# Kernel tuning notes

Measured on AMD Instinct MI355X. Metric: run time of the kernel, lower is better.

## Reference

```python
import jax, jax.numpy as jnp
import numpy as np

N_NODES = 100000
N_EDGES = 1600000
IN_DIM = 128
OUT_DIM = 32
N_HEADS = 4


def setup_inputs() -> dict:
    key = jax.random.key(0)
    k1, k2, k3, k4, k5 = jax.random.split(key, 5)
    x = jax.random.normal(k1, (N_NODES, IN_DIM), dtype=jnp.float32)
    edge_index = jax.random.randint(k2, (2, N_EDGES), 0, N_NODES, dtype=jnp.int64)
    # torch nn.Linear weight layout: [out_features, in_features]
    W = jax.random.normal(k3, (OUT_DIM * N_HEADS, IN_DIM), dtype=jnp.float32) * (1.0 / np.sqrt(IN_DIM))
    a_left = jax.random.normal(k4, (N_HEADS, OUT_DIM), dtype=jnp.float32) * 0.01
    a_right = jax.random.normal(k5, (N_HEADS, OUT_DIM), dtype=jnp.float32) * 0.01
    return {"x": x, "edge_index": edge_index, "W": W, "a_left": a_left, "a_right": a_right}


def reference(x, edge_index, W, a_left, a_right):
    N = x.shape[0]
    H, D = a_left.shape
    # h: [N, H, D]
    h = (x @ W.T).reshape(N, H, D)
    src = edge_index[0]
    dst = edge_index[1]
    h_src = h[src]                                   # [E, H, D] gather
    h_dst = h[dst]                                   # [E, H, D] gather
    e = jnp.einsum('ehd,hd->eh', h_src, a_left) + jnp.einsum('ehd,hd->eh', h_dst, a_right)
    e = jax.nn.leaky_relu(e, negative_slope=0.2)
    e_exp = jnp.exp(e)                               # faithful: no max-subtraction, as in source
    denom = jax.ops.segment_sum(e_exp, dst, num_segments=N)   # [N, H]
    alpha = e_exp / (denom[dst] + 1e-8)              # [E, H]
    weighted = h_src * alpha[:, :, None]             # [E, H, D]
    out = jax.ops.segment_sum(weighted, dst, num_segments=N)  # [N, H, D]
    return out.reshape(N, H * D)                     # concat=True
```

## Files before the change

kernel.cpp:

```cpp
#include <hip/hip_runtime.h>
#include <hip/hip_bf16.h>


constexpr int IN_DIM = 128;
constexpr int HD     = 128;
constexpr int CSHIFT = 9;
constexpr int CCAP   = 9216;
constexpr int CPAD   = 16;

typedef float f32x4 __attribute__((ext_vector_type(4)));
typedef short short8 __attribute__((ext_vector_type(8)));

__device__ __forceinline__ unsigned short f2bf(float f) {
  __hip_bfloat16 b = __float2bfloat16(f);
  return *(unsigned short*)&b;
}
__device__ __forceinline__ float bfl(unsigned u) { return __uint_as_float(u << 16); }
__device__ __forceinline__ float bfh(unsigned u) { return __uint_as_float(u & 0xffff0000u); }

__device__ __forceinline__
void gemm_role(char* xs, int gb_idx,
               const float* __restrict__ x, const float* __restrict__ W,
               const float* __restrict__ a_left, const float* __restrict__ a_right,
               unsigned int* __restrict__ hb,
               float* __restrict__ el, float* __restrict__ er, int N) {
  const int tid  = threadIdx.x;
  const int lane = tid & 63;
  const int wv   = tid >> 6;
  const int lcol = lane & 15;
  const int lk   = lane >> 4;
  const int n0   = gb_idx * 64;

  short8 Bh[2][4], Bl[2][4];
#pragma unroll
  for (int ct = 0; ct < 2; ++ct) {
    int col = wv * 32 + ct * 16 + lcol;
#pragma unroll
    for (int ks = 0; ks < 4; ++ks) {
      int kb = ks * 32 + lk * 8;
      const float* wp = &W[col * IN_DIM + kb];
      float4 wa = *(const float4*)wp;
      float4 wb = *(const float4*)(wp + 4);
      float wf[8] = {wa.x, wa.y, wa.z, wa.w, wb.x, wb.y, wb.z, wb.w};
      short8 uh, ul;
#pragma unroll
      for (int j = 0; j < 8; ++j) {
        unsigned short hs = f2bf(wf[j]);
        float hf = __uint_as_float((unsigned)hs << 16);
        uh[j] = (short)hs;
        ul[j] = (short)f2bf(wf[j] - hf);
      }
      Bh[ct][ks] = uh;  Bl[ct][ks] = ul;
    }
  }

#pragma unroll
  for (int i = 0; i < 8; ++i) {
    int f  = tid + 256 * i;
    int r  = f >> 5;
    int c4 = f & 31;
    int node = n0 + r;
    float4 v = make_float4(0.f, 0.f, 0.f, 0.f);
    if (node < N) v = *(const float4*)&x[(size_t)node * IN_DIM + c4 * 4];
    float vf[4] = {v.x, v.y, v.z, v.w};
    unsigned short hs[4], ls[4];
#pragma unroll
    for (int j = 0; j < 4; ++j) {
      hs[j] = f2bf(vf[j]);
      float hf = __uint_as_float((unsigned)hs[j] << 16);
      ls[j] = f2bf(vf[j] - hf);
    }
    int sw = (c4 * 8) ^ ((r & 7) << 4);
    uint2 ph = make_uint2((unsigned)hs[0] | ((unsigned)hs[1] << 16),
                          (unsigned)hs[2] | ((unsigned)hs[3] << 16));
    uint2 pl = make_uint2((unsigned)ls[0] | ((unsigned)ls[1] << 16),
                          (unsigned)ls[2] | ((unsigned)ls[3] << 16));
    *(uint2*)&xs[r * 256 + sw]         = ph;
    *(uint2*)&xs[16384 + r * 256 + sw] = pl;
  }
  __syncthreads();

  f32x4 acc[4][2];
#pragma unroll
  for (int rt = 0; rt < 4; ++rt)
#pragma unroll
    for (int ct = 0; ct < 2; ++ct) acc[rt][ct] = (f32x4){0.f, 0.f, 0.f, 0.f};

#pragma unroll
  for (int ks = 0; ks < 4; ++ks) {
#pragma unroll
    for (int rt = 0; rt < 4; ++rt) {
      int row = rt * 16 + lcol;
      int kb  = ks * 64 + lk * 16;
      int ad  = row * 256 + (kb ^ ((row & 7) << 4));
      short8 ah = *(const short8*)&xs[ad];
      short8 al = *(const short8*)&xs[16384 + ad];
#pragma unroll
      for (int ct = 0; ct < 2; ++ct) {
        acc[rt][ct] = __builtin_amdgcn_mfma_f32_16x16x32_bf16(ah, Bh[ct][ks], acc[rt][ct], 0, 0, 0);
        acc[rt][ct] = __builtin_amdgcn_mfma_f32_16x16x32_bf16(ah, Bl[ct][ks], acc[rt][ct], 0, 0, 0);
        acc[rt][ct] = __builtin_amdgcn_mfma_f32_16x16x32_bf16(al, Bh[ct][ks], acc[rt][ct], 0, 0, 0);
      }
    }
  }

  float aL[2], aR[2];
  aL[0] = a_left [wv * 32 + lcol];  aL[1] = a_left [wv * 32 + 16 + lcol];
  aR[0] = a_right[wv * 32 + lcol];  aR[1] = a_right[wv * 32 + 16 + lcol];

#pragma unroll
  for (int rt = 0; rt < 4; ++rt) {
    float pl[4] = {0.f, 0.f, 0.f, 0.f}, pr[4] = {0.f, 0.f, 0.f, 0.f};
#pragma unroll
    for (int ct = 0; ct < 2; ++ct) {
      float av[4] = {acc[rt][ct][0], acc[rt][ct][1], acc[rt][ct][2], acc[rt][ct][3]};
      float pt[4];
#pragma unroll
      for (int r = 0; r < 4; ++r) pt[r] = __shfl_xor(av[r], 1, 64);
      int col = wv * 32 + ct * 16 + lcol;
      int nb  = n0 + rt * 16 + lk * 4;
      if (!(lane & 1)) {
#pragma unroll
        for (int r = 0; r < 4; ++r) {
          int node = nb + r;
          if (node < N)
            hb[(size_t)node * 64 + (col >> 1)] =
                (unsigned)f2bf(av[r]) | ((unsigned)f2bf(pt[r]) << 16);
        }
      }
#pragma unroll
      for (int r = 0; r < 4; ++r) { pl[r] += av[r] * aL[ct]; pr[r] += av[r] * aR[ct]; }
    }
#pragma unroll
    for (int m = 1; m < 16; m <<= 1)
#pragma unroll
      for (int r = 0; r < 4; ++r) {
        pl[r] += __shfl_xor(pl[r], m, 64);
        pr[r] += __shfl_xor(pr[r], m, 64);
      }
    if (lcol == 0) {
#pragma unroll
      for (int r = 0; r < 4; ++r) {
        int node = n0 + rt * 16 + lk * 4 + r;
        if (node < N) { el[node * 4 + wv] = pl[r]; er[node * 4 + wv] = pr[r]; }
      }
    }
  }
}

__device__ __forceinline__
void binA_role(char* smem, int ab_idx,
               const int* __restrict__ ei, int* __restrict__ ccnt,
               unsigned* __restrict__ c1buf, int E, int ncb) {
  unsigned*       staged = (unsigned*)smem;
  unsigned short* sbin   = (unsigned short*)(smem + 8192);
  int*            hist   = (int*)(smem + 12288);
  int*            loff   = (int*)(smem + 13312);
  int*            cur    = (int*)(smem + 14336);
  int*            gbase  = (int*)(smem + 15360);
  int*            lws    = (int*)(smem + 16384);
  const int t = threadIdx.x;
  const int base = ab_idx * 2048;

  hist[t] = 0;
  __syncthreads();

  int src[8], dst[8], bin[8];
#pragma unroll
  for (int i = 0; i < 8; ++i) {
    int e = base + t + 256 * i;
    if (e < E) {
      src[i] = __builtin_nontemporal_load(&ei[e]);
      dst[i] = __builtin_nontemporal_load(&ei[E + e]);
      bin[i] = dst[i] >> CSHIFT;
      atomicAdd(&hist[bin[i]], 1);
    } else bin[i] = -1;
  }
  __syncthreads();

  int v = hist[t], s = v;
#pragma unroll
  for (int d = 1; d < 64; d <<= 1) {
    int u = __shfl_up(s, d, 64);
    if ((t & 63) >= d) s += u;
  }
  if ((t & 63) == 63) lws[t >> 6] = s;
  __syncthreads();
  int prefix = 0;
  for (int i = 0; i < (t >> 6); ++i) prefix += lws[i];
  int excl = prefix + s - v;
  loff[t] = excl;
  cur[t]  = excl;
  gbase[t] = (t < ncb && v > 0) ? atomicAdd(&ccnt[t * CPAD], v) : 0;
  __syncthreads();

#pragma unroll
  for (int i = 0; i < 8; ++i) {
    if (bin[i] >= 0) {
      int p = atomicAdd(&cur[bin[i]], 1);
      staged[p] = (unsigned)src[i] | ((unsigned)(dst[i] & 511) << 17);
      sbin[p]   = (unsigned short)bin[i];
    }
  }
  __syncthreads();

  const int tot = loff[255] + hist[255];
  for (int j = t; j < tot; j += 256) {
    int b = sbin[j];
    int pos = gbase[b] + (j - loff[b]);
    if (pos < CCAP) c1buf[(size_t)b * CCAP + pos] = staged[j];
  }
}

__global__ __launch_bounds__(256)
void fused_k(const float* __restrict__ x, const float* __restrict__ W,
             const float* __restrict__ a_left, const float* __restrict__ a_right,
             unsigned int* __restrict__ hb, float* __restrict__ el,
             float* __restrict__ er, const int* __restrict__ ei,
             int* __restrict__ ccnt, unsigned* __restrict__ c1buf,
             int N, int E, int ncb, int nab) {
  __shared__ __align__(16) char smem[32768];
  const int k = blockIdx.x;
  const int twoA = 2 * nab;
  if (k < twoA && (k & 1)) {
    binA_role(smem, k >> 1, ei, ccnt, c1buf, E, ncb);
  } else {
    int gidx = (k < twoA) ? (k >> 1) : (k - nab);
    gemm_role(smem, gidx, x, W, a_left, a_right, hb, el, er, N);
  }
}

__global__ __launch_bounds__(512)
void binB_k(const unsigned* __restrict__ c1buf, const int* __restrict__ ccnt,
            int* __restrict__ offsets, int* __restrict__ csr,
            int N, int ncb, int E) {
  __shared__ int hist[512];
  __shared__ int wsum[8];
  __shared__ int lws2[4];
  __shared__ int sgb;
  const int b = blockIdx.x, t = threadIdx.x;

  hist[t] = 0;

  int cv = 0, cs = 0;
  if (t < 256) {
    cv = (t < ncb) ? ccnt[t * CPAD] : 0;
    cs = cv;
#pragma unroll
    for (int d = 1; d < 64; d <<= 1) {
      int u = __shfl_up(cs, d, 64);
      if ((t & 63) >= d) cs += u;
    }
    if ((t & 63) == 63) lws2[t >> 6] = cs;
  }
  if (t == 0 && b == 0) offsets[N] = E;
  __syncthreads();
  if (t < 256) {
    int cpre = 0;
    for (int i = 0; i < (t >> 6); ++i) cpre += lws2[i];
    if (t == b) sgb = cpre + cs - cv;
  }
  __syncthreads();
  const int gb = sgb;

  int m = ccnt[b * CPAD];
  if (m > CCAP) m = CCAP;
  const unsigned* bp = c1buf + (size_t)b * CCAP;
  for (int i = t; i < m; i += 512) atomicAdd(&hist[bp[i] >> 17], 1);
  __syncthreads();

  int v = hist[t], s = v;
#pragma unroll
  for (int d = 1; d < 64; d <<= 1) {
    int u = __shfl_up(s, d, 64);
    if ((t & 63) >= d) s += u;
  }
  if ((t & 63) == 63) wsum[t >> 6] = s;
  __syncthreads();
  int prefix = 0;
  for (int w = 0; w < (t >> 6); ++w) prefix += wsum[w];
  int excl = prefix + s - v;
  int node = (b << CSHIFT) + t;
  if (node < N) offsets[node] = gb + excl;
  hist[t] = excl;
  __syncthreads();

  for (int i = t; i < m; i += 512) {
    unsigned u = bp[i];
    int r = atomicAdd(&hist[u >> 17], 1);
    csr[gb + r] = (int)(u & 0x1FFFFu);
  }
}

__global__ __launch_bounds__(256)
void agg_k(const char* __restrict__ hbc, const char* __restrict__ elc,
           const float* __restrict__ er, const int* __restrict__ offsets,
           const int* __restrict__ csr, float* __restrict__ out, int N) {
  const int wid  = (blockIdx.x * blockDim.x + threadIdx.x) >> 6;
  const int lane = threadIdx.x & 63;
  if (wid >= N) return;
  const int start = offsets[wid];
  const int end   = offsets[wid + 1];
  const int q    = lane >> 4;
  const int ql   = lane & 15;
  const int head = ql >> 2;
  const unsigned qoff = (unsigned)(ql << 4);
  const unsigned hoff = (unsigned)(head << 2);
  const float erv = er[wid * 4 + head];

  float a0=0.f,a1=0.f,a2=0.f,a3=0.f,a4=0.f,a5=0.f,a6=0.f,a7=0.f,den=0.f;

  for (int base = start; base < end; base += 64) {
    int lim = end - base; if (lim > 64) lim = 64;
    int ce  = base + lane;
    int creg = __builtin_nontemporal_load(&csr[(ce < end) ? ce : (end - 1)]);

    int i = 0;
    for (; i + 8 <= lim; i += 8) {
      int s0 = __shfl(creg, i + q, 64);
      int s1 = __shfl(creg, i + 4 + q, 64);
      uint4 h0 = *(const uint4*)(hbc + (((unsigned)s0 << 8) + qoff));
      uint4 h1 = *(const uint4*)(hbc + (((unsigned)s1 << 8) + qoff));
      float e0 = *(const float*)(elc + (((unsigned)s0 << 4) + hoff));
      float e1 = *(const float*)(elc + (((unsigned)s1 << 4) + hoff));
      float t0 = e0 + erv; t0 = (t0 > 0.f) ? t0 : 0.2f * t0;
      float t1 = e1 + erv; t1 = (t1 > 0.f) ? t1 : 0.2f * t1;
      float w0 = __expf(t0), w1 = __expf(t1);
      a0 += w0 * bfl(h0.x) + w1 * bfl(h1.x);
      a1 += w0 * bfh(h0.x) + w1 * bfh(h1.x);
      a2 += w0 * bfl(h0.y) + w1 * bfl(h1.y);
      a3 += w0 * bfh(h0.y) + w1 * bfh(h1.y);
      a4 += w0 * bfl(h0.z) + w1 * bfl(h1.z);
      a5 += w0 * bfh(h0.z) + w1 * bfh(h1.z);
      a6 += w0 * bfl(h0.w) + w1 * bfl(h1.w);
      a7 += w0 * bfh(h0.w) + w1 * bfh(h1.w);
      den += w0 + w1;
    }
    if (i < lim) {
      int i0 = i + q, i1 = i + 4 + q;
      int s0 = __shfl(creg, (i0 < lim) ? i0 : 0, 64);
      int s1 = __shfl(creg, (i1 < lim) ? i1 : 0, 64);
      uint4 h0 = *(const uint4*)(hbc + (((unsigned)s0 << 8) + qoff));
      uint4 h1 = *(const uint4*)(hbc + (((unsigned)s1 << 8) + qoff));
      float e0 = *(const float*)(elc + (((unsigned)s0 << 4) + hoff));
      float e1 = *(const float*)(elc + (((unsigned)s1 << 4) + hoff));
      float t0 = e0 + erv; t0 = (t0 > 0.f) ? t0 : 0.2f * t0;
      float t1 = e1 + erv; t1 = (t1 > 0.f) ? t1 : 0.2f * t1;
      float w0 = __expf(t0), w1 = __expf(t1);
      if (i0 >= lim) w0 = 0.f;
      if (i1 >= lim) w1 = 0.f;
      a0 += w0 * bfl(h0.x) + w1 * bfl(h1.x);
      a1 += w0 * bfh(h0.x) + w1 * bfh(h1.x);
      a2 += w0 * bfl(h0.y) + w1 * bfl(h1.y);
      a3 += w0 * bfh(h0.y) + w1 * bfh(h1.y);
      a4 += w0 * bfl(h0.z) + w1 * bfl(h1.z);
      a5 += w0 * bfh(h0.z) + w1 * bfh(h1.z);
      a6 += w0 * bfl(h0.w) + w1 * bfl(h1.w);
      a7 += w0 * bfh(h0.w) + w1 * bfh(h1.w);
      den += w0 + w1;
    }
  }

#pragma unroll
  for (int m = 16; m < 64; m <<= 1) {
    a0 += __shfl_xor(a0, m, 64);  a1 += __shfl_xor(a1, m, 64);
    a2 += __shfl_xor(a2, m, 64);  a3 += __shfl_xor(a3, m, 64);
    a4 += __shfl_xor(a4, m, 64);  a5 += __shfl_xor(a5, m, 64);
    a6 += __shfl_xor(a6, m, 64);  a7 += __shfl_xor(a7, m, 64);
    den += __shfl_xor(den, m, 64);
  }
  if (q == 0) {
    float inv = 1.f / (den + 1e-8f);
    f32x4 o0 = {a0 * inv, a1 * inv, a2 * inv, a3 * inv};
    f32x4 o1 = {a4 * inv, a5 * inv, a6 * inv, a7 * inv};
    __builtin_nontemporal_store(o0, (f32x4*)&out[(size_t)wid * HD + 8 * ql]);
    __builtin_nontemporal_store(o1, (f32x4*)&out[(size_t)wid * HD + 8 * ql + 4]);
  }
}

extern "C" void kernel_launch(void* const* d_in, const int* in_sizes, int n_in,
                              void* d_out, int out_size, void* d_ws, size_t ws_size,
                              hipStream_t stream) {
  const float* x       = (const float*)d_in[0];
  const int*   ei      = (const int*)d_in[1];
  const float* W       = (const float*)d_in[2];
  const float* a_left  = (const float*)d_in[3];
  const float* a_right = (const float*)d_in[4];
  float* out = (float*)d_out;

  const int N = in_sizes[0] / IN_DIM;
  const int E = in_sizes[1] / 2;
  const int NCB = (N + (1 << CSHIFT) - 1) >> CSHIFT;
  const int GB  = (N + 63) / 64;
  const int AB  = (E + 2047) / 2048;

  char* p = (char*)d_ws;
  unsigned int* hb = (unsigned int*)p; p += (size_t)N * 64 * sizeof(unsigned int);
  float* el      = (float*)p; p += (size_t)N * 4 * sizeof(float);
  float* er      = (float*)p; p += (size_t)N * 4 * sizeof(float);
  int*   offsets = (int*)p;   p += (size_t)(N + 1) * sizeof(int);
  int*   ccnt    = (int*)p;   p += (size_t)256 * CPAD * sizeof(int);
  int*   csr     = (int*)p;   p += (size_t)E * sizeof(int);
  unsigned* c1buf = (unsigned*)p; p += (size_t)NCB * CCAP * sizeof(unsigned);

  hipMemsetAsync(ccnt, 0, (size_t)256 * CPAD * sizeof(int), stream);

  fused_k<<<GB + AB, 256, 0, stream>>>(x, W, a_left, a_right, hb, el, er,
                                       ei, ccnt, c1buf, N, E, NCB, AB);
  binB_k<<<NCB, 512, 0, stream>>>(c1buf, ccnt, offsets, csr, N, NCB, E);
  agg_k<<<(N + 3) / 4, 256, 0, stream>>>((const char*)hb, (const char*)el, er,
                                         offsets, csr, out, N);
}
```

Before: 234.4 us.

## Precompute bf16 split of W and fold attention vectors into extra GEMM columns

```diff
diff --git a/kernel.cpp b/kernel.cpp
--- a/kernel.cpp
+++ b/kernel.cpp
@@ -7,6 +7,7 @@
 constexpr int CSHIFT = 9;
 constexpr int CCAP   = 9216;
 constexpr int CPAD   = 16;
+constexpr int WCOLS  = 144;
 
 typedef float f32x4 __attribute__((ext_vector_type(4)));
 typedef short short8 __attribute__((ext_vector_type(8)));
@@ -18,10 +19,46 @@
 __device__ __forceinline__ float bfl(unsigned u) { return __uint_as_float(u << 16); }
 __device__ __forceinline__ float bfh(unsigned u) { return __uint_as_float(u & 0xffff0000u); }
 
+__global__ __launch_bounds__(1024)
+void prep_k(const float* __restrict__ W, const float* __restrict__ a_left,
+            const float* __restrict__ a_right,
+            unsigned short* __restrict__ Whb, unsigned short* __restrict__ Wlb,
+            int* __restrict__ ccnt) {
+  const int t = threadIdx.x;
+  for (int i = t; i < 256 * CPAD; i += 1024) ccnt[i] = 0;
+
+  for (int i = t; i < 128 * 128; i += 1024) {
+    float w = W[i];
+    unsigned wu = __float_as_uint(w);
+    unsigned short h = (unsigned short)(wu >> 16);
+    float hf = __uint_as_float(wu & 0xffff0000u);
+    Whb[i] = h;
+    Wlb[i] = f2bf(w - hf);
+  }
+  {
+    int vec = t >> 7;
+    int k   = t & 127;
+    int hd  = vec & 3;
+    const float* av = (vec < 4) ? a_left : a_right;
+    float s = 0.f;
+    for (int d = 0; d < 32; ++d) s += av[hd * 32 + d] * W[(hd * 32 + d) * IN_DIM + k];
+    unsigned su = __float_as_uint(s);
+    unsigned short h = (unsigned short)(su >> 16);
+    float hf = __uint_as_float(su & 0xffff0000u);
+    Whb[(128 + vec) * 128 + k] = h;
+    Wlb[(128 + vec) * 128 + k] = f2bf(s - hf);
+  }
+  for (int i = t; i < 8 * 128; i += 1024) {
+    Whb[136 * 128 + i] = 0;
+    Wlb[136 * 128 + i] = 0;
+  }
+}
+
 __device__ __forceinline__
 void gemm_role(char* xs, int gb_idx,
-               const float* __restrict__ x, const float* __restrict__ W,
-               const float* __restrict__ a_left, const float* __restrict__ a_right,
+               const float* __restrict__ x,
+               const unsigned short* __restrict__ Whb,
+               const unsigned short* __restrict__ Wlb,
                unsigned int* __restrict__ hb,
                float* __restrict__ el, float* __restrict__ er, int N) {
   const int tid  = threadIdx.x;
@@ -30,29 +67,6 @@
   const int lcol = lane & 15;
   const int lk   = lane >> 4;
   const int n0   = gb_idx * 64;
-
-  short8 Bh[2][4], Bl[2][4];
-#pragma unroll
-  for (int ct = 0; ct < 2; ++ct) {
-    int col = wv * 32 + ct * 16 + lcol;
-#pragma unroll
-    for (int ks = 0; ks < 4; ++ks) {
-      int kb = ks * 32 + lk * 8;
-      const float* wp = &W[col * IN_DIM + kb];
-      float4 wa = *(const float4*)wp;
-      float4 wb = *(const float4*)(wp + 4);
-      float wf[8] = {wa.x, wa.y, wa.z, wa.w, wb.x, wb.y, wb.z, wb.w};
-      short8 uh, ul;
-#pragma unroll
-      for (int j = 0; j < 8; ++j) {
-        unsigned short hs = f2bf(wf[j]);
-        float hf = __uint_as_float((unsigned)hs << 16);
-        uh[j] = (short)hs;
-        ul[j] = (short)f2bf(wf[j] - hf);
-      }
-      Bh[ct][ks] = uh;  Bl[ct][ks] = ul;
-    }
-  }
 
 #pragma unroll
   for (int i = 0; i < 8; ++i) {
@@ -66,8 +80,9 @@
     unsigned short hs[4], ls[4];
 #pragma unroll
     for (int j = 0; j < 4; ++j) {
-      hs[j] = f2bf(vf[j]);
-      float hf = __uint_as_float((unsigned)hs[j] << 16);
+      unsigned xu = __float_as_uint(vf[j]);
+      hs[j] = (unsigned short)(xu >> 16);
+      float hf = __uint_as_float(xu & 0xffff0000u);
       ls[j] = f2bf(vf[j] - hf);
     }
     int sw = (c4 * 8) ^ ((r & 7) << 4);
@@ -81,36 +96,49 @@
   __syncthreads();
 
   f32x4 acc[4][2];
-#pragma unroll
-  for (int rt = 0; rt < 4; ++rt)
-#pragma unroll
-    for (int ct = 0; ct < 2; ++ct) acc[rt][ct] = (f32x4){0.f, 0.f, 0.f, 0.f};
+  f32x4 acc2[4];
+#pragma unroll
+  for (int rt = 0; rt < 4; ++rt) {
+    acc[rt][0] = (f32x4){0.f, 0.f, 0.f, 0.f};
+    acc[rt][1] = (f32x4){0.f, 0.f, 0.f, 0.f};
+    acc2[rt]   = (f32x4){0.f, 0.f, 0.f, 0.f};
+  }
 
 #pragma unroll
   for (int ks = 0; ks < 4; ++ks) {
+    const int kb = ks * 32 + lk * 8;
+    short8 bh0 = *(const short8*)&Whb[(size_t)(wv * 32 + lcol) * 128 + kb];
+    short8 bl0 = *(const short8*)&Wlb[(size_t)(wv * 32 + lcol) * 128 + kb];
+    short8 bh1 = *(const short8*)&Whb[(size_t)(wv * 32 + 16 + lcol) * 128 + kb];
+    short8 bl1 = *(const short8*)&Wlb[(size_t)(wv * 32 + 16 + lcol) * 128 + kb];
+    short8 bh2 = {}, bl2 = {};
+    if (wv == 0) {
+      bh2 = *(const short8*)&Whb[(size_t)(128 + lcol) * 128 + kb];
+      bl2 = *(const short8*)&Wlb[(size_t)(128 + lcol) * 128 + kb];
+    }
 #pragma unroll
     for (int rt = 0; rt < 4; ++rt) {
       int row = rt * 16 + lcol;
-      int kb  = ks * 64 + lk * 16;
-      int ad  = row * 256 + (kb ^ ((row & 7) << 4));
+      int kbyte = ks * 64 + lk * 16;
+      int ad  = row * 256 + (kbyte ^ ((row & 7) << 4));
       short8 ah = *(const short8*)&xs[ad];
       short8 al = *(const short8*)&xs[16384 + ad];
-#pragma unroll
-      for (int ct = 0; ct < 2; ++ct) {
-        acc[rt][ct] = __builtin_amdgcn_mfma_f32_16x16x32_bf16(ah, Bh[ct][ks], acc[rt][ct], 0, 0, 0);
-        acc[rt][ct] = __builtin_amdgcn_mfma_f32_16x16x32_bf16(ah, Bl[ct][ks], acc[rt][ct], 0, 0, 0);
-        acc[rt][ct] = __builtin_amdgcn_mfma_f32_16x16x32_bf16(al, Bh[ct][ks], acc[rt][ct], 0, 0, 0);
+      acc[rt][0] = __builtin_amdgcn_mfma_f32_16x16x32_bf16(ah, bh0, acc[rt][0], 0, 0, 0);
+      acc[rt][0] = __builtin_amdgcn_mfma_f32_16x16x32_bf16(ah, bl0, acc[rt][0], 0, 0, 0);
+      acc[rt][0] = __builtin_amdgcn_mfma_f32_16x16x32_bf16(al, bh0, acc[rt][0], 0, 0, 0);
+      acc[rt][1] = __builtin_amdgcn_mfma_f32_16x16x32_bf16(ah, bh1, acc[rt][1], 0, 0, 0);
+      acc[rt][1] = __builtin_amdgcn_mfma_f32_16x16x32_bf16(ah, bl1, acc[rt][1], 0, 0, 0);
+      acc[rt][1] = __builtin_amdgcn_mfma_f32_16x16x32_bf16(al, bh1, acc[rt][1], 0, 0, 0);
+      if (wv == 0) {
+        acc2[rt] = __builtin_amdgcn_mfma_f32_16x16x32_bf16(ah, bh2, acc2[rt], 0, 0, 0);
+        acc2[rt] = __builtin_amdgcn_mfma_f32_16x16x32_bf16(ah, bl2, acc2[rt], 0, 0, 0);
+        acc2[rt] = __builtin_amdgcn_mfma_f32_16x16x32_bf16(al, bh2, acc2[rt], 0, 0, 0);
       }
     }
   }
 
-  float aL[2], aR[2];
-  aL[0] = a_left [wv * 32 + lcol];  aL[1] = a_left [wv * 32 + 16 + lcol];
-  aR[0] = a_right[wv * 32 + lcol];  aR[1] = a_right[wv * 32 + 16 + lcol];
-
 #pragma unroll
   for (int rt = 0; rt < 4; ++rt) {
-    float pl[4] = {0.f, 0.f, 0.f, 0.f}, pr[4] = {0.f, 0.f, 0.f, 0.f};
 #pragma unroll
     for (int ct = 0; ct < 2; ++ct) {
       float av[4] = {acc[rt][ct][0], acc[rt][ct][1], acc[rt][ct][2], acc[rt][ct][3]};
@@ -128,21 +156,15 @@
                 (unsigned)f2bf(av[r]) | ((unsigned)f2bf(pt[r]) << 16);
         }
       }
-#pragma unroll
-      for (int r = 0; r < 4; ++r) { pl[r] += av[r] * aL[ct]; pr[r] += av[r] * aR[ct]; }
-    }
-#pragma unroll
-    for (int m = 1; m < 16; m <<= 1)
+    }
+    if (wv == 0 && lcol < 8) {
+      float* dstp = (lcol < 4) ? el : er;
+      int hd = lcol & 3;
+      int nb = n0 + rt * 16 + lk * 4;
 #pragma unroll
       for (int r = 0; r < 4; ++r) {
-        pl[r] += __shfl_xor(pl[r], m, 64);
-        pr[r] += __shfl_xor(pr[r], m, 64);
-      }
-    if (lcol == 0) {
-#pragma unroll
-      for (int r = 0; r < 4; ++r) {
-        int node = n0 + rt * 16 + lk * 4 + r;
-        if (node < N) { el[node * 4 + wv] = pl[r]; er[node * 4 + wv] = pr[r]; }
+        int node = nb + r;
+        if (node < N) dstp[node * 4 + hd] = acc2[rt][r];
       }
     }
   }
@@ -213,8 +235,9 @@
 }
 
 __global__ __launch_bounds__(256)
-void fused_k(const float* __restrict__ x, const float* __restrict__ W,
-             const float* __restrict__ a_left, const float* __restrict__ a_right,
+void fused_k(const float* __restrict__ x,
+             const unsigned short* __restrict__ Whb,
+             const unsigned short* __restrict__ Wlb,
              unsigned int* __restrict__ hb, float* __restrict__ el,
              float* __restrict__ er, const int* __restrict__ ei,
              int* __restrict__ ccnt, unsigned* __restrict__ c1buf,
@@ -226,7 +249,7 @@
     binA_role(smem, k >> 1, ei, ccnt, c1buf, E, ncb);
   } else {
     int gidx = (k < twoA) ? (k >> 1) : (k - nab);
-    gemm_role(smem, gidx, x, W, a_left, a_right, hb, el, er, N);
+    gemm_role(smem, gidx, x, Whb, Wlb, hb, el, er, N);
   }
 }
 
@@ -398,14 +421,15 @@
   unsigned int* hb = (unsigned int*)p; p += (size_t)N * 64 * sizeof(unsigned int);
   float* el      = (float*)p; p += (size_t)N * 4 * sizeof(float);
   float* er      = (float*)p; p += (size_t)N * 4 * sizeof(float);
-  int*   offsets = (int*)p;   p += (size_t)(N + 1) * sizeof(int);
+  int*   offsets = (int*)p;   p += (size_t)(N + 4) * sizeof(int);
   int*   ccnt    = (int*)p;   p += (size_t)256 * CPAD * sizeof(int);
+  unsigned short* Whb = (unsigned short*)p; p += (size_t)WCOLS * 128 * sizeof(unsigned short);
+  unsigned short* Wlb = (unsigned short*)p; p += (size_t)WCOLS * 128 * sizeof(unsigned short);
   int*   csr     = (int*)p;   p += (size_t)E * sizeof(int);
   unsigned* c1buf = (unsigned*)p; p += (size_t)NCB * CCAP * sizeof(unsigned);
 
-  hipMemsetAsync(ccnt, 0, (size_t)256 * CPAD * sizeof(int), stream);
-
-  fused_k<<<GB + AB, 256, 0, stream>>>(x, W, a_left, a_right, hb, el, er,
+  prep_k<<<1, 1024, 0, stream>>>(W, a_left, a_right, Whb, Wlb, ccnt);
+  fused_k<<<GB + AB, 256, 0, stream>>>(x, Whb, Wlb, hb, el, er,
                                        ei, ccnt, c1buf, N, E, NCB, AB);
   binB_k<<<NCB, 512, 0, stream>>>(c1buf, ccnt, offsets, csr, N, NCB, E);
   agg_k<<<(N + 3) / 4, 256, 0, stream>>>((const char*)hb, (const char*)el, er,
```

New measurement: 232.5 us. About the same (-0.8%).
